# Optimization experiments

Measured on AMD Instinct MI355X. Metric: run time of the kernel, lower is better.

The kernel has to match this reference:

```python
import jax, jax.numpy as jnp
import numpy as np

B, N, D, H = 4, 8192, 1024, 16
HD = D // H  # head dim 64
EPS = 1e-5


def setup_inputs() -> dict:
    key = jax.random.key(0)
    ks = jax.random.split(key, 12)
    s = 1.0 / np.sqrt(D)
    return {
        "query": jax.random.normal(ks[0], (B, N, D), jnp.float32),
        "Wq": jax.random.normal(ks[1], (D, D), jnp.float32) * s,
        "bq": jax.random.normal(ks[2], (D,), jnp.float32) * 0.01,
        "Wk": jax.random.normal(ks[3], (D, D), jnp.float32) * s,
        "bk": jax.random.normal(ks[4], (D,), jnp.float32) * 0.01,
        "Wv": jax.random.normal(ks[5], (D, D), jnp.float32) * s,
        "bv": jax.random.normal(ks[6], (D,), jnp.float32) * 0.01,
        "Wu": jax.random.normal(ks[7], (D, D), jnp.float32) * s,
        "bu": jax.random.normal(ks[8], (D,), jnp.float32) * 0.01,
        "Wo": jax.random.normal(ks[9], (D, D), jnp.float32) * s,
        "bo": jax.random.normal(ks[10], (D,), jnp.float32) * 0.01,
        "ln_w": jnp.ones((D,), jnp.float32),
        "ln_b": jnp.zeros((D,), jnp.float32),
    }


def _abs_clamp(t, min_mag=0.01, max_mag=100.0):
    return jnp.clip(jnp.abs(t), min_mag, max_mag) * jnp.sign(t)


def _heads(x):  # [b, n, h*d] -> [b, h, n, d]
    b, n, _ = x.shape
    return x.reshape(b, n, H, HD).transpose(0, 2, 1, 3)


def reference(query, Wq, bq, Wk, bk, Wv, bv, Wu, bu, Wo, bo, ln_w, ln_b):
    q = jax.nn.relu(_heads(query @ Wq + bq))  # [b,h,n,d]
    k = jax.nn.relu(_heads(query @ Wk + bk))
    v = _heads(query @ Wv + bv)
    u = query @ Wu + bu  # [b,n,D]
    # global linear-attention reduction: kv[b,h,d,e] = sum_n k v
    kv = jnp.einsum('bhnd,bhne->bhde', k, v)
    kv = _abs_clamp(kv)
    out = jnp.einsum('bhnd,bhde->bhne', q, kv)  # [b,h,n,d]
    out = out.transpose(0, 2, 1, 3).reshape(query.shape)  # [b,n,D]
    # LayerNorm over last dim
    mu = jnp.mean(out, axis=-1, keepdims=True)
    var = jnp.var(out, axis=-1, keepdims=True)
    out = (out - mu) * jax.lax.rsqrt(var + EPS) * ln_w + ln_b
    out = u * out
    return out @ Wo + bo
```

## Files before the change

### kernel.cpp

```cpp
#include <hip/hip_runtime.h>

#define M_TOT 32768

typedef float f32x4 __attribute__((ext_vector_type(4)));
typedef short s16x8 __attribute__((ext_vector_type(8)));

#define AS1(p) ((__attribute__((address_space(1))) void*)(p))
#define AS3(p) ((__attribute__((address_space(3))) void*)(p))

#define BARRIER() asm volatile("s_barrier" ::: "memory")
#define VMCNT4() asm volatile("s_waitcnt vmcnt(4)" ::: "memory")
#define VMCNT2() asm volatile("s_waitcnt vmcnt(2)" ::: "memory")
#define VMCNT0() asm volatile("s_waitcnt vmcnt(0)" ::: "memory")

__device__ __forceinline__ short f2bf(float f) {
    unsigned u = __builtin_bit_cast(unsigned, f);
    u += 0x7fffu + ((u >> 16) & 1u);
    return (short)(u >> 16);
}
__device__ __forceinline__ float bf2f(short s) {
    unsigned u = ((unsigned)(unsigned short)s) << 16;
    return __builtin_bit_cast(float, u);
}

__global__ void conv_x(const float* __restrict__ x, short* __restrict__ y) {
    const size_t nchunk = (size_t)M_TOT * 1024 / 8;
    const size_t stride = (size_t)gridDim.x * blockDim.x;
    for (size_t c = (size_t)blockIdx.x * blockDim.x + threadIdx.x; c < nchunk; c += stride) {
        const float4* src = (const float4*)(x + c * 8);
        float4 a = src[0], b = src[1];
        s16x8 r;
        r[0] = f2bf(a.x); r[1] = f2bf(a.y); r[2] = f2bf(a.z); r[3] = f2bf(a.w);
        r[4] = f2bf(b.x); r[5] = f2bf(b.y); r[6] = f2bf(b.z); r[7] = f2bf(b.w);
        *(s16x8*)(y + c * 8) = r;
    }
}

__global__ __launch_bounds__(256) void conv_w(const float* __restrict__ Wq,
                                              const float* __restrict__ Wk,
                                              const float* __restrict__ Wv,
                                              const float* __restrict__ Wu,
                                              const float* __restrict__ Wo,
                                              short* __restrict__ Wcat) {
    __shared__ float t[64][65];
    const int b = blockIdx.x;
    const int mat = b >> 8;
    const int kt = (b >> 4) & 15, nt = b & 15;
    const int k0 = kt << 6, n0 = nt << 6;
    const float* W = (mat == 0) ? Wq : (mat == 1) ? Wk : (mat == 2) ? Wv
                   : (mat == 3) ? Wu : Wo;
    const int rr = threadIdx.x >> 4;
    const int cc = threadIdx.x & 15;
    #pragma unroll
    for (int p = 0; p < 4; ++p) {
        const int row = p * 16 + rr;
        const float4 v = *(const float4*)(W + (size_t)(k0 + row) * 1024 + n0 + cc * 4);
        t[row][cc * 4 + 0] = v.x; t[row][cc * 4 + 1] = v.y;
        t[row][cc * 4 + 2] = v.z; t[row][cc * 4 + 3] = v.w;
    }
    __syncthreads();
    #pragma unroll
    for (int p = 0; p < 4; ++p) {
        const int nr = p * 16 + rr;
        short4 r;
        r.x = f2bf(t[cc * 4 + 0][nr]); r.y = f2bf(t[cc * 4 + 1][nr]);
        r.z = f2bf(t[cc * 4 + 2][nr]); r.w = f2bf(t[cc * 4 + 3][nr]);
        *(short4*)(Wcat + (size_t)(mat * 1024 + n0 + nr) * 1024 + k0 + cc * 4) = r;
    }
}

__global__ void conv_bias(const float* __restrict__ bq, const float* __restrict__ bk,
                          const float* __restrict__ bv, const float* __restrict__ bu,
                          const float* __restrict__ bo, float* __restrict__ bcat) {
    const int i = blockIdx.x * 256 + threadIdx.x;
    const float* b = (i < 1024) ? bq : (i < 2048) ? bk : (i < 3072) ? bv
                   : (i < 4096) ? bu : bo;
    bcat[i] = b[i & 1023];
}

template <int MODE>
__global__ __launch_bounds__(512, 2) void gemm8(
        const short* __restrict__ A, const short* __restrict__ W,
        const float* __restrict__ bias,
        short* __restrict__ qb, short* __restrict__ ktb,
        short* __restrict__ vtb, short* __restrict__ ub,
        float* __restrict__ outb) {
    extern __shared__ char lds[];
    const int tid = threadIdx.x;
    const int wave = tid >> 6, lane = tid & 63;
    const int r16 = lane & 15, g = lane >> 4;
    const int moff = (wave >> 2) << 7;
    const int noff = (wave & 3) << 6;

    const int nwg = (MODE == 0) ? 2048 : 512;
    const int NB = (MODE == 0) ? 16 : 4;
    const int bid = blockIdx.x;
    const int swz = (bid & 7) * (nwg >> 3) + (bid >> 3);
    const int mblk = swz / NB, nblk = swz % NB;
    const int row0 = mblk << 8, col0 = nblk << 8;

    const int rswz = r16 & 7;
    const int ck0 = (g ^ rswz) << 4;
    const int ck1 = ((4 + g) ^ rswz) << 4;
    const int rowbA = (moff + r16) << 7;
    const int rowbB = (noff + r16) << 7;

    const char* baseA = (const char*)A + (size_t)(row0 + wave * 8 + (lane >> 3)) * 2048
                        + (((lane & 7) ^ ((lane >> 3) & 7)) << 4);
    const char* baseB = (const char*)W + (size_t)(col0 + wave * 8 + (lane >> 3)) * 2048
                        + (((lane & 7) ^ ((lane >> 3) & 7)) << 4);

#define STG(BASE, J, T, DST)                                                   \
    __builtin_amdgcn_global_load_lds(                                          \
        AS1((BASE) + (size_t)(J) * 131072 + (size_t)(T) * 128),                \
        AS3((DST) + (J) * 8192 + wave * 1024), 16, 0, 0)

#define RDA(V, M, BUFA) {                                                      \
    (V)[0] = *(const s16x8*)((BUFA) + rowbA + (M) * 2048 + ck0);               \
    (V)[1] = *(const s16x8*)((BUFA) + rowbA + (M) * 2048 + ck1); }

#define RDB(V, N, BUFB) {                                                      \
    (V)[0] = *(const s16x8*)((BUFB) + rowbB + (N) * 2048 + ck0);               \
    (V)[1] = *(const s16x8*)((BUFB) + rowbB + (N) * 2048 + ck1); }

#define MF16(P, A0, A1)                                                        \
    _Pragma("unroll") for (int kk = 0; kk < 2; ++kk)                           \
        _Pragma("unroll") for (int n = 0; n < 4; ++n) {                        \
            acc[2*(P)][n]   = __builtin_amdgcn_mfma_f32_16x16x32_bf16((A0)[kk], bfr[n][kk], acc[2*(P)][n], 0, 0, 0);   \
            acc[2*(P)+1][n] = __builtin_amdgcn_mfma_f32_16x16x32_bf16((A1)[kk], bfr[n][kk], acc[2*(P)+1][n], 0, 0, 0); \
        }

#define TILE(T, DOSTAGE, TRmid, TRend) {                                       \
    char* bA_ = lds + ((T) & 1) * 65536; char* bB_ = bA_ + 32768;              \
    char* sA_ = lds + (((T) + 1) & 1) * 65536; char* sB_ = sA_ + 32768;        \
    s16x8 a0[2], a1[2], a2[2], a3[2];                                          \
    if (DOSTAGE) { STG(baseB, 0, (T) + 1, sB_); STG(baseB, 1, (T) + 1, sB_);   \
                   STG(baseB, 2, (T) + 1, sB_); STG(baseB, 3, (T) + 1, sB_); } \
    _Pragma("unroll") for (int n = 0; n < 4; ++n) RDB(bfr[n], n, bB_);         \
    RDA(a0, 0, bA_); RDA(a1, 1, bA_); RDA(a2, 2, bA_); RDA(a3, 3, bA_);        \
    __builtin_amdgcn_s_setprio(1);                                             \
    MF16(0, a0, a1); MF16(1, a2, a3);                                          \
    __builtin_amdgcn_s_setprio(0);                                             \
    TRmid; BARRIER();                                                          \
    if (DOSTAGE) { STG(baseA, 0, (T) + 1, sA_); STG(baseA, 2, (T) + 1, sA_);   \
                   STG(baseA, 1, (T) + 1, sA_); STG(baseA, 3, (T) + 1, sA_); } \
    RDA(a0, 4, bA_); RDA(a1, 5, bA_); RDA(a2, 6, bA_); RDA(a3, 7, bA_);        \
    __builtin_amdgcn_s_setprio(1);                                             \
    MF16(2, a0, a1); MF16(3, a2, a3);                                          \
    __builtin_amdgcn_s_setprio(0);                                             \
    TRend; BARRIER(); }

    f32x4 acc[8][4] = {};
    s16x8 bfr[4][2];

    STG(baseB, 0, 0, lds + 32768); STG(baseB, 1, 0, lds + 32768);
    STG(baseB, 2, 0, lds + 32768); STG(baseB, 3, 0, lds + 32768);
    STG(baseA, 0, 0, lds);         STG(baseA, 2, 0, lds);
    STG(baseA, 1, 0, lds);         STG(baseA, 3, 0, lds);
    VMCNT2();
    BARRIER();

    #pragma unroll 1
    for (int t = 0; t < 15; ++t) TILE(t, true, VMCNT4(), VMCNT2());
    TILE(15, false, VMCNT0(), (void)0);

    const int rj = (lane >> 4) << 2;
    if (MODE == 1) {
        #pragma unroll
        for (int n = 0; n < 4; ++n) {
            const int gn = col0 + noff + n * 16 + r16;
            const float bv = bias[gn];
            #pragma unroll
            for (int m = 0; m < 8; ++m) {
                const int gm0 = row0 + moff + m * 16 + rj;
                #pragma unroll
                for (int j = 0; j < 4; ++j)
                    outb[(size_t)(gm0 + j) * 1024 + gn] = acc[m][n][j] + bv;
            }
        }
    } else {
        const int seg = col0 >> 10;
        if (seg == 0 || seg == 3) {
            short* dst = (seg == 0) ? qb : ub;
            const bool do_relu = (seg == 0);
            #pragma unroll
            for (int n = 0; n < 4; ++n) {
                const int gn = col0 + noff + n * 16 + r16;
                const int f = gn & 1023;
                const float bv = bias[gn];
                #pragma unroll
                for (int m = 0; m < 8; ++m) {
                    const int gm0 = row0 + moff + m * 16 + rj;
                    #pragma unroll
                    for (int j = 0; j < 4; ++j) {
                        float val = acc[m][n][j] + bv;
                        if (do_relu) val = fmaxf(val, 0.0f);
                        dst[(size_t)(gm0 + j) * 1024 + f] = f2bf(val);
                    }
                }
            }
        } else {
            short* dst = (seg == 1) ? ktb : vtb;
            const bool do_relu = (seg == 1);
            #pragma unroll
            for (int n = 0; n < 4; ++n) {
                const int gn = col0 + noff + n * 16 + r16;
                const int hd = gn & 1023;
                const float bv = bias[gn];
                #pragma unroll
                for (int m = 0; m < 8; ++m) {
                    const int gm0 = row0 + moff + m * 16 + rj;
                    const int b = gm0 >> 13;
                    const int ntok = gm0 & 8191;
                    float v0 = acc[m][n][0] + bv, v1 = acc[m][n][1] + bv;
                    float v2 = acc[m][n][2] + bv, v3 = acc[m][n][3] + bv;
                    if (do_relu) {
                        v0 = fmaxf(v0, 0.0f); v1 = fmaxf(v1, 0.0f);
                        v2 = fmaxf(v2, 0.0f); v3 = fmaxf(v3, 0.0f);
                    }
                    short4 pk;
                    pk.x = f2bf(v0); pk.y = f2bf(v1); pk.z = f2bf(v2); pk.w = f2bf(v3);
                    *(short4*)(dst + ((size_t)(b * 1024 + hd)) * 8192 + ntok) = pk;
                }
            }
        }
    }
#undef TILE
#undef MF16
#undef RDB
#undef RDA
#undef STG
}

__global__ __launch_bounds__(256) void kv_partial(const short* __restrict__ ktb,
                                                  const short* __restrict__ vtb,
                                                  float* __restrict__ kvp) {
    __shared__ float red[4][4096];
    const int slice = blockIdx.x;
    const int bh = blockIdx.y;
    const int wave = threadIdx.x >> 6, lane = threadIdx.x & 63;
    const int r16 = lane & 15;
    const short* kb = ktb + (size_t)bh * 64 * 8192;
    const short* vb = vtb + (size_t)bh * 64 * 8192;
    const int n0 = (slice << 10) + (wave << 8);
    f32x4 acc[4][4] = {};
    for (int s = 0; s < 8; ++s) {
        const int nk = n0 + (s << 5) + ((lane >> 4) << 3);
        s16x8 af[4], bf[4];
        #pragma unroll
        for (int m = 0; m < 4; ++m) af[m] = *(const s16x8*)(kb + (size_t)(m * 16 + r16) * 8192 + nk);
        #pragma unroll
        for (int n = 0; n < 4; ++n) bf[n] = *(const s16x8*)(vb + (size_t)(n * 16 + r16) * 8192 + nk);
        #pragma unroll
        for (int m = 0; m < 4; ++m)
            #pragma unroll
            for (int n = 0; n < 4; ++n)
                acc[m][n] = __builtin_amdgcn_mfma_f32_16x16x32_bf16(af[m], bf[n], acc[m][n], 0, 0, 0);
    }
    const int rj = (lane >> 4) << 2;
    #pragma unroll
    for (int m = 0; m < 4; ++m)
        #pragma unroll
        for (int n = 0; n < 4; ++n)
            #pragma unroll
            for (int j = 0; j < 4; ++j)
                red[wave][(m * 16 + rj + j) * 64 + n * 16 + r16] = acc[m][n][j];
    __syncthreads();
    float* dst = kvp + ((size_t)slice * 64 + bh) * 4096;
    const int i0 = threadIdx.x * 16;
    #pragma unroll
    for (int e = 0; e < 16; e += 4) {
        f32x4 a0 = *(const f32x4*)&red[0][i0 + e];
        f32x4 a1 = *(const f32x4*)&red[1][i0 + e];
        f32x4 a2 = *(const f32x4*)&red[2][i0 + e];
        f32x4 a3 = *(const f32x4*)&red[3][i0 + e];
        *(f32x4*)&dst[i0 + e] = (a0 + a1) + (a2 + a3);
    }
}

__global__ void kv_reduce(const float* __restrict__ kvp, short* __restrict__ kvt) {
    const int bh = blockIdx.x;
    for (int i = threadIdx.x; i < 4096; i += 256) {
        float s = 0.0f;
        #pragma unroll
        for (int sl = 0; sl < 8; ++sl)
            s += kvp[((size_t)sl * 64 + bh) * 4096 + i];
        float a = fabsf(s);
        float cmag = fminf(fmaxf(a, 0.01f), 100.0f);
        float r = (s > 0.0f) ? cmag : ((s < 0.0f) ? -cmag : 0.0f);
        const int d = i >> 6, e = i & 63;
        kvt[(size_t)bh * 4096 + e * 64 + d] = f2bf(r);
    }
}

__global__ __launch_bounds__(256) void qkv_ln(const short* __restrict__ qb,
                                              const short* __restrict__ kvt,
                                              const short* __restrict__ ub,
                                              const float* __restrict__ lnw,
                                              const float* __restrict__ lnb,
                                              short* __restrict__ yb) {
    __shared__ short tr[4][1024];
    const int wave = threadIdx.x >> 6, lane = threadIdx.x & 63;
    const int r16 = lane & 15, g = lane >> 4;
    const size_t rowB = (size_t)blockIdx.x * 64 + wave * 16;
    const int bh0 = (int)((rowB >> 13) << 4);
    const short* qrow = qb + (rowB + r16) * 1024 + g * 8;

    float s[4] = {0, 0, 0, 0}, sq[4] = {0, 0, 0, 0};
    for (int h = 0; h < 16; ++h) {
        const short* kvb = kvt + (size_t)(bh0 + h) * 4096 + g * 8;
        f32x4 a4[4] = {};
        #pragma unroll
        for (int kk = 0; kk < 2; ++kk) {
            const s16x8 af = *(const s16x8*)(qrow + h * 64 + kk * 32);
            #pragma unroll
            for (int n = 0; n < 4; ++n) {
                const s16x8 bf = *(const s16x8*)(kvb + (n * 16 + r16) * 64 + kk * 32);
                a4[n] = __builtin_amdgcn_mfma_f32_16x16x32_bf16(af, bf, a4[n], 0, 0, 0);
            }
        }
        #pragma unroll
        for (int n = 0; n < 4; ++n)
            #pragma unroll
            for (int j = 0; j < 4; ++j) {
                const float v = a4[n][j];
                s[j] += v; sq[j] += v * v;
            }
    }
    #pragma unroll
    for (int j = 0; j < 4; ++j) {
        #pragma unroll
        for (int mk = 1; mk < 16; mk <<= 1) {
            s[j] += __shfl_xor(s[j], mk);
            sq[j] += __shfl_xor(sq[j], mk);
        }
    }
    float mu[4], rs[4];
    #pragma unroll
    for (int j = 0; j < 4; ++j) {
        mu[j] = s[j] * (1.0f / 1024.0f);
        const float var = sq[j] * (1.0f / 1024.0f) - mu[j] * mu[j];
        rs[j] = rsqrtf(var + 1e-5f);
    }

    short* trw = &tr[wave][0];
    const int rdr = lane >> 3;
    const int c0 = (lane & 7) * 8;
    for (int h = 0; h < 16; ++h) {
        const short* kvb = kvt + (size_t)(bh0 + h) * 4096 + g * 8;
        f32x4 a4[4] = {};
        #pragma unroll
        for (int kk = 0; kk < 2; ++kk) {
            const s16x8 af = *(const s16x8*)(qrow + h * 64 + kk * 32);
            #pragma unroll
            for (int n = 0; n < 4; ++n) {
                const s16x8 bf = *(const s16x8*)(kvb + (n * 16 + r16) * 64 + kk * 32);
                a4[n] = __builtin_amdgcn_mfma_f32_16x16x32_bf16(af, bf, a4[n], 0, 0, 0);
            }
        }
        #pragma unroll
        for (int n = 0; n < 4; ++n) {
            const float lw = lnw[h * 64 + n * 16 + r16];
            const float lb = lnb[h * 64 + n * 16 + r16];
            #pragma unroll
            for (int j = 0; j < 4; ++j) {
                const float val = (a4[n][j] - mu[j]) * rs[j] * lw + lb;
                trw[(g * 4 + j) * 64 + ((n ^ g) * 16 + r16)] = f2bf(val);
            }
        }
        #pragma unroll
        for (int p = 0; p < 2; ++p) {
            const int r = rdr + p * 8;
            const s16x8 t = *(const s16x8*)&trw[r * 64 + (((c0 >> 4) ^ (r >> 2)) * 16) + (c0 & 15)];
            const s16x8 uu = *(const s16x8*)(ub + (rowB + r) * 1024 + h * 64 + c0);
            s16x8 o;
            #pragma unroll
            for (int e = 0; e < 8; ++e)
                o[e] = f2bf(bf2f(t[e]) * bf2f(uu[e]));
            *(s16x8*)(yb + (rowB + r) * 1024 + h * 64 + c0) = o;
        }
    }
}

extern "C" void kernel_launch(void* const* d_in, const int* in_sizes, int n_in,
                              void* d_out, int out_size, void* d_ws, size_t ws_size,
                              hipStream_t stream) {
    (void)in_sizes; (void)n_in; (void)out_size;
    const float* query = (const float*)d_in[0];
    const float* Wq = (const float*)d_in[1];
    const float* bq = (const float*)d_in[2];
    const float* Wk = (const float*)d_in[3];
    const float* bk = (const float*)d_in[4];
    const float* Wv = (const float*)d_in[5];
    const float* bv = (const float*)d_in[6];
    const float* Wu = (const float*)d_in[7];
    const float* bu = (const float*)d_in[8];
    const float* Wo = (const float*)d_in[9];
    const float* bo = (const float*)d_in[10];
    const float* lnw = (const float*)d_in[11];
    const float* lnb = (const float*)d_in[12];
    float* out = (float*)d_out;
    char* ws = (char*)d_ws;
    if (ws_size < 380129280u) return;

    short* Xb   = (short*)(ws);
    short* Wcat = (short*)(ws + 67108864);
    float* bcat = (float*)(ws + 77594624);
    short* qb   = (short*)(ws + 77615104);
    short* ktb  = (short*)(ws + 144723968);
    short* vtb  = (short*)(ws + 211832832);
    short* ub   = (short*)(ws + 278941696);
    float* kvp  = (float*)(ws + 346050560);
    short* kvt  = (short*)(ws + 379604992);
    short* yb   = Xb;

    hipFuncSetAttribute(reinterpret_cast<const void*>(&gemm8<0>),
                        hipFuncAttributeMaxDynamicSharedMemorySize, 131072);
    hipFuncSetAttribute(reinterpret_cast<const void*>(&gemm8<1>),
                        hipFuncAttributeMaxDynamicSharedMemorySize, 131072);

    conv_x<<<2048, 256, 0, stream>>>(query, Xb);
    conv_w<<<1280, 256, 0, stream>>>(Wq, Wk, Wv, Wu, Wo, Wcat);
    conv_bias<<<20, 256, 0, stream>>>(bq, bk, bv, bu, bo, bcat);
    gemm8<0><<<2048, 512, 131072, stream>>>(Xb, Wcat, bcat, qb, ktb, vtb, ub, nullptr);
    kv_partial<<<dim3(8, 64), 256, 0, stream>>>(ktb, vtb, kvp);
    kv_reduce<<<64, 256, 0, stream>>>(kvp, kvt);
    qkv_ln<<<512, 256, 0, stream>>>(qb, kvt, ub, lnw, lnb, yb);
    gemm8<1><<<512, 512, 131072, stream>>>(yb, Wcat + (size_t)4096 * 1024, bcat + 4096,
                                           nullptr, nullptr, nullptr, nullptr, out);
}
```

Before: 537.4 us.

## Restructure GEMM main loop into four k-split phases with interleaved staging

The GEMM inner loop now splits each 64-wide K tile into four phases by M-half and K-half, holding only one K-slice of A and B fragments in registers at a time. Each phase issues its LDS reads and two global-to-LDS stage loads, then waits on a barrier and lgkmcnt(0) before running 16 MFMAs under raised priority. The goal is to spread global loads more evenly across the tile and to cut fragment register pressure. In exchange it adds two extra barriers per tile and full LDS waits that may expose read latency.

```diff
diff --git a/kernel.cpp b/kernel.cpp
--- a/kernel.cpp
+++ b/kernel.cpp
@@ -9,7 +9,7 @@
 #define AS3(p) ((__attribute__((address_space(3))) void*)(p))
 
 #define BARRIER() asm volatile("s_barrier" ::: "memory")
-#define VMCNT4() asm volatile("s_waitcnt vmcnt(4)" ::: "memory")
+#define LGKM0()  asm volatile("s_waitcnt lgkmcnt(0)" ::: "memory")
 #define VMCNT2() asm volatile("s_waitcnt vmcnt(2)" ::: "memory")
 #define VMCNT0() asm volatile("s_waitcnt vmcnt(0)" ::: "memory")
 
@@ -79,7 +79,7 @@
 }
 
 template <int MODE>
-__global__ __launch_bounds__(512, 2) void gemm8(
+__global__ __launch_bounds__(512, 2) void gemm9(
         const short* __restrict__ A, const short* __restrict__ W,
         const float* __restrict__ bias,
         short* __restrict__ qb, short* __restrict__ ktb,
@@ -115,54 +115,58 @@
         AS1((BASE) + (size_t)(J) * 131072 + (size_t)(T) * 128),                \
         AS3((DST) + (J) * 8192 + wave * 1024), 16, 0, 0)
 
-#define RDA(V, M, BUFA) {                                                      \
-    (V)[0] = *(const s16x8*)((BUFA) + rowbA + (M) * 2048 + ck0);               \
-    (V)[1] = *(const s16x8*)((BUFA) + rowbA + (M) * 2048 + ck1); }
-
-#define RDB(V, N, BUFB) {                                                      \
-    (V)[0] = *(const s16x8*)((BUFB) + rowbB + (N) * 2048 + ck0);               \
-    (V)[1] = *(const s16x8*)((BUFB) + rowbB + (N) * 2048 + ck1); }
-
-#define MF16(P, A0, A1)                                                        \
-    _Pragma("unroll") for (int kk = 0; kk < 2; ++kk)                           \
-        _Pragma("unroll") for (int n = 0; n < 4; ++n) {                        \
-            acc[2*(P)][n]   = __builtin_amdgcn_mfma_f32_16x16x32_bf16((A0)[kk], bfr[n][kk], acc[2*(P)][n], 0, 0, 0);   \
-            acc[2*(P)+1][n] = __builtin_amdgcn_mfma_f32_16x16x32_bf16((A1)[kk], bfr[n][kk], acc[2*(P)+1][n], 0, 0, 0); \
-        }
-
-#define TILE(T, DOSTAGE, TRmid, TRend) {                                       \
-    char* bA_ = lds + ((T) & 1) * 65536; char* bB_ = bA_ + 32768;              \
-    char* sA_ = lds + (((T) + 1) & 1) * 65536; char* sB_ = sA_ + 32768;        \
-    s16x8 a0[2], a1[2], a2[2], a3[2];                                          \
-    if (DOSTAGE) { STG(baseB, 0, (T) + 1, sB_); STG(baseB, 1, (T) + 1, sB_);   \
-                   STG(baseB, 2, (T) + 1, sB_); STG(baseB, 3, (T) + 1, sB_); } \
-    _Pragma("unroll") for (int n = 0; n < 4; ++n) RDB(bfr[n], n, bB_);         \
-    RDA(a0, 0, bA_); RDA(a1, 1, bA_); RDA(a2, 2, bA_); RDA(a3, 3, bA_);        \
+#define RA(M, QM, CK) (*(const s16x8*)(bA_ + rowbA + (QM) * 8192 + (M) * 2048 + (CK)))
+#define RB(N, CK)     (*(const s16x8*)(bB_ + rowbB + (N) * 2048 + (CK)))
+
+#define PH(QM, CK, FRESHB, DOST, SBASE, J1, J2, SDST, WAITOP) {                \
+    afr[0] = RA(0, QM, CK); afr[1] = RA(1, QM, CK);                            \
+    afr[2] = RA(2, QM, CK); afr[3] = RA(3, QM, CK);                            \
+    if (FRESHB) { bfr[0] = RB(0, CK); bfr[1] = RB(1, CK);                      \
+                  bfr[2] = RB(2, CK); bfr[3] = RB(3, CK); }                    \
+    if (DOST) { STG(SBASE, J1, tt + 1, SDST); STG(SBASE, J2, tt + 1, SDST); }  \
+    BARRIER();                                                                 \
+    LGKM0();                                                                   \
+    __builtin_amdgcn_sched_barrier(0);                                         \
     __builtin_amdgcn_s_setprio(1);                                             \
-    MF16(0, a0, a1); MF16(1, a2, a3);                                          \
+    _Pragma("unroll") for (int m = 0; m < 4; ++m)                              \
+        _Pragma("unroll") for (int n = 0; n < 4; ++n)                          \
+            acc[(QM) * 4 + m][n] = __builtin_amdgcn_mfma_f32_16x16x32_bf16(    \
+                afr[m], bfr[n], acc[(QM) * 4 + m][n], 0, 0, 0);                \
     __builtin_amdgcn_s_setprio(0);                                             \
-    TRmid; BARRIER();                                                          \
-    if (DOSTAGE) { STG(baseA, 0, (T) + 1, sA_); STG(baseA, 2, (T) + 1, sA_);   \
-                   STG(baseA, 1, (T) + 1, sA_); STG(baseA, 3, (T) + 1, sA_); } \
-    RDA(a0, 4, bA_); RDA(a1, 5, bA_); RDA(a2, 6, bA_); RDA(a3, 7, bA_);        \
-    __builtin_amdgcn_s_setprio(1);                                             \
-    MF16(2, a0, a1); MF16(3, a2, a3);                                          \
-    __builtin_amdgcn_s_setprio(0);                                             \
-    TRend; BARRIER(); }
+    WAITOP;                                                                    \
+    BARRIER(); }
 
     f32x4 acc[8][4] = {};
-    s16x8 bfr[4][2];
-
-    STG(baseB, 0, 0, lds + 32768); STG(baseB, 1, 0, lds + 32768);
-    STG(baseB, 2, 0, lds + 32768); STG(baseB, 3, 0, lds + 32768);
-    STG(baseA, 0, 0, lds);         STG(baseA, 2, 0, lds);
-    STG(baseA, 1, 0, lds);         STG(baseA, 3, 0, lds);
+    s16x8 afr[4], bfr[4];
+
+    {
+        const int tt = -1;
+        STG(baseB, 0, tt + 1, lds + 32768); STG(baseB, 1, tt + 1, lds + 32768);
+        STG(baseB, 2, tt + 1, lds + 32768); STG(baseB, 3, tt + 1, lds + 32768);
+        STG(baseA, 0, tt + 1, lds);         STG(baseA, 2, tt + 1, lds);
+        STG(baseA, 1, tt + 1, lds);         STG(baseA, 3, tt + 1, lds);
+    }
     VMCNT2();
     BARRIER();
 
     #pragma unroll 1
-    for (int t = 0; t < 15; ++t) TILE(t, true, VMCNT4(), VMCNT2());
-    TILE(15, false, VMCNT0(), (void)0);
+    for (int tt = 0; tt < 15; ++tt) {
+        char* bA_ = lds + (tt & 1) * 65536; char* bB_ = bA_ + 32768;
+        char* sA_ = lds + ((tt + 1) & 1) * 65536; char* sB_ = sA_ + 32768;
+        PH(0, ck0, true,  true, baseB, 0, 1, sB_, VMCNT2());
+        PH(1, ck0, false, true, baseB, 2, 3, sB_, (void)0);
+        PH(0, ck1, true,  true, baseA, 0, 2, sA_, (void)0);
+        PH(1, ck1, false, true, baseA, 1, 3, sA_, VMCNT2());
+    }
+    {
+        const int tt = 15;
+        char* bA_ = lds + (tt & 1) * 65536; char* bB_ = bA_ + 32768;
+        char* sA_ = nullptr; char* sB_ = nullptr; (void)sA_; (void)sB_;
+        PH(0, ck0, true,  false, baseB, 0, 1, sB_, VMCNT0());
+        PH(1, ck0, false, false, baseB, 2, 3, sB_, (void)0);
+        PH(0, ck1, true,  false, baseA, 0, 2, sA_, (void)0);
+        PH(1, ck1, false, false, baseA, 1, 3, sA_, (void)0);
+    }
 
     const int rj = (lane >> 4) << 2;
     if (MODE == 1) {
@@ -225,10 +229,9 @@
             }
         }
     }
-#undef TILE
-#undef MF16
-#undef RDB
-#undef RDA
+#undef PH
+#undef RB
+#undef RA
 #undef STG
 }
 
@@ -414,18 +417,18 @@
     short* kvt  = (short*)(ws + 379604992);
     short* yb   = Xb;
 
-    hipFuncSetAttribute(reinterpret_cast<const void*>(&gemm8<0>),
+    hipFuncSetAttribute(reinterpret_cast<const void*>(&gemm9<0>),
                         hipFuncAttributeMaxDynamicSharedMemorySize, 131072);
-    hipFuncSetAttribute(reinterpret_cast<const void*>(&gemm8<1>),
+    hipFuncSetAttribute(reinterpret_cast<const void*>(&gemm9<1>),
                         hipFuncAttributeMaxDynamicSharedMemorySize, 131072);
 
     conv_x<<<2048, 256, 0, stream>>>(query, Xb);
     conv_w<<<1280, 256, 0, stream>>>(Wq, Wk, Wv, Wu, Wo, Wcat);
     conv_bias<<<20, 256, 0, stream>>>(bq, bk, bv, bu, bo, bcat);
-    gemm8<0><<<2048, 512, 131072, stream>>>(Xb, Wcat, bcat, qb, ktb, vtb, ub, nullptr);
+    gemm9<0><<<2048, 512, 131072, stream>>>(Xb, Wcat, bcat, qb, ktb, vtb, ub, nullptr);
     kv_partial<<<dim3(8, 64), 256, 0, stream>>>(ktb, vtb, kvp);
     kv_reduce<<<64, 256, 0, stream>>>(kvp, kvt);
     qkv_ln<<<512, 256, 0, stream>>>(qb, kvt, ub, lnw, lnb, yb);
-    gemm8<1><<<512, 512, 131072, stream>>>(yb, Wcat + (size_t)4096 * 1024, bcat + 4096,
+    gemm9<1><<<512, 512, 131072, stream>>>(yb, Wcat + (size_t)4096 * 1024, bcat + 4096,
                                            nullptr, nullptr, nullptr, nullptr, out);
 }
```

Result: no change. 542.2 us (+0.9%).

## Triple-buffer GEMM with K=32 tiles and merge prep kernels into one launch

Applied to the files above, without the earlier changes.

The main GEMM changes from a two-stage pipeline with K=64 tiles (128 KB LDS) to a three-stage ring of K=32 tiles (96 KB LDS), prefetching two tiles ahead. It uses a new XOR swizzle and a single barrier per tile. The three conversion kernels (x, weights, bias) are merged into one prep launch to cut launch overhead. Risks: twice as many barriers over the K loop, and lower MFMA work per synchronization.

```diff
diff --git a/kernel.cpp b/kernel.cpp
--- a/kernel.cpp
+++ b/kernel.cpp
@@ -10,7 +10,6 @@
 
 #define BARRIER() asm volatile("s_barrier" ::: "memory")
 #define VMCNT4() asm volatile("s_waitcnt vmcnt(4)" ::: "memory")
-#define VMCNT2() asm volatile("s_waitcnt vmcnt(2)" ::: "memory")
 #define VMCNT0() asm volatile("s_waitcnt vmcnt(0)" ::: "memory")
 
 __device__ __forceinline__ short f2bf(float f) {
@@ -23,63 +22,61 @@
     return __builtin_bit_cast(float, u);
 }
 
-__global__ void conv_x(const float* __restrict__ x, short* __restrict__ y) {
-    const size_t nchunk = (size_t)M_TOT * 1024 / 8;
-    const size_t stride = (size_t)gridDim.x * blockDim.x;
-    for (size_t c = (size_t)blockIdx.x * blockDim.x + threadIdx.x; c < nchunk; c += stride) {
-        const float4* src = (const float4*)(x + c * 8);
-        float4 a = src[0], b = src[1];
-        s16x8 r;
-        r[0] = f2bf(a.x); r[1] = f2bf(a.y); r[2] = f2bf(a.z); r[3] = f2bf(a.w);
-        r[4] = f2bf(b.x); r[5] = f2bf(b.y); r[6] = f2bf(b.z); r[7] = f2bf(b.w);
-        *(s16x8*)(y + c * 8) = r;
-    }
-}
-
-__global__ __launch_bounds__(256) void conv_w(const float* __restrict__ Wq,
-                                              const float* __restrict__ Wk,
-                                              const float* __restrict__ Wv,
-                                              const float* __restrict__ Wu,
-                                              const float* __restrict__ Wo,
-                                              short* __restrict__ Wcat) {
+__global__ __launch_bounds__(256) void prep(const float* __restrict__ x, short* __restrict__ y,
+                                            const float* __restrict__ Wq, const float* __restrict__ Wk,
+                                            const float* __restrict__ Wv, const float* __restrict__ Wu,
+                                            const float* __restrict__ Wo, short* __restrict__ Wcat,
+                                            const float* __restrict__ bq, const float* __restrict__ bk,
+                                            const float* __restrict__ bv, const float* __restrict__ bu,
+                                            const float* __restrict__ bo, float* __restrict__ bcat) {
     __shared__ float t[64][65];
-    const int b = blockIdx.x;
-    const int mat = b >> 8;
-    const int kt = (b >> 4) & 15, nt = b & 15;
-    const int k0 = kt << 6, n0 = nt << 6;
-    const float* W = (mat == 0) ? Wq : (mat == 1) ? Wk : (mat == 2) ? Wv
-                   : (mat == 3) ? Wu : Wo;
-    const int rr = threadIdx.x >> 4;
-    const int cc = threadIdx.x & 15;
-    #pragma unroll
-    for (int p = 0; p < 4; ++p) {
-        const int row = p * 16 + rr;
-        const float4 v = *(const float4*)(W + (size_t)(k0 + row) * 1024 + n0 + cc * 4);
-        t[row][cc * 4 + 0] = v.x; t[row][cc * 4 + 1] = v.y;
-        t[row][cc * 4 + 2] = v.z; t[row][cc * 4 + 3] = v.w;
-    }
-    __syncthreads();
-    #pragma unroll
-    for (int p = 0; p < 4; ++p) {
-        const int nr = p * 16 + rr;
-        short4 r;
-        r.x = f2bf(t[cc * 4 + 0][nr]); r.y = f2bf(t[cc * 4 + 1][nr]);
-        r.z = f2bf(t[cc * 4 + 2][nr]); r.w = f2bf(t[cc * 4 + 3][nr]);
-        *(short4*)(Wcat + (size_t)(mat * 1024 + n0 + nr) * 1024 + k0 + cc * 4) = r;
-    }
-}
-
-__global__ void conv_bias(const float* __restrict__ bq, const float* __restrict__ bk,
-                          const float* __restrict__ bv, const float* __restrict__ bu,
-                          const float* __restrict__ bo, float* __restrict__ bcat) {
-    const int i = blockIdx.x * 256 + threadIdx.x;
-    const float* b = (i < 1024) ? bq : (i < 2048) ? bk : (i < 3072) ? bv
-                   : (i < 4096) ? bu : bo;
-    bcat[i] = b[i & 1023];
+    const int blk = blockIdx.x;
+    if (blk < 2048) {
+        const size_t nchunk = (size_t)M_TOT * 1024 / 8;
+        const size_t stride = (size_t)2048 * 256;
+        for (size_t c = (size_t)blk * 256 + threadIdx.x; c < nchunk; c += stride) {
+            const float4* src = (const float4*)(x + c * 8);
+            float4 a = src[0], b = src[1];
+            s16x8 r;
+            r[0] = f2bf(a.x); r[1] = f2bf(a.y); r[2] = f2bf(a.z); r[3] = f2bf(a.w);
+            r[4] = f2bf(b.x); r[5] = f2bf(b.y); r[6] = f2bf(b.z); r[7] = f2bf(b.w);
+            *(s16x8*)(y + c * 8) = r;
+        }
+    } else if (blk < 3328) {
+        const int b = blk - 2048;
+        const int mat = b >> 8;
+        const int kt = (b >> 4) & 15, nt = b & 15;
+        const int k0 = kt << 6, n0 = nt << 6;
+        const float* W = (mat == 0) ? Wq : (mat == 1) ? Wk : (mat == 2) ? Wv
+                       : (mat == 3) ? Wu : Wo;
+        const int rr = threadIdx.x >> 4;
+        const int cc = threadIdx.x & 15;
+        #pragma unroll
+        for (int p = 0; p < 4; ++p) {
+            const int row = p * 16 + rr;
+            const float4 v = *(const float4*)(W + (size_t)(k0 + row) * 1024 + n0 + cc * 4);
+            t[row][cc * 4 + 0] = v.x; t[row][cc * 4 + 1] = v.y;
+            t[row][cc * 4 + 2] = v.z; t[row][cc * 4 + 3] = v.w;
+        }
+        __syncthreads();
+        #pragma unroll
+        for (int p = 0; p < 4; ++p) {
+            const int nr = p * 16 + rr;
+            short4 r;
+            r.x = f2bf(t[cc * 4 + 0][nr]); r.y = f2bf(t[cc * 4 + 1][nr]);
+            r.z = f2bf(t[cc * 4 + 2][nr]); r.w = f2bf(t[cc * 4 + 3][nr]);
+            *(short4*)(Wcat + (size_t)(mat * 1024 + n0 + nr) * 1024 + k0 + cc * 4) = r;
+        }
+    } else {
+        const int i = (blk - 3328) * 256 + threadIdx.x;
+        const float* b = (i < 1024) ? bq : (i < 2048) ? bk : (i < 3072) ? bv
+                       : (i < 4096) ? bu : bo;
+        bcat[i] = b[i & 1023];
+    }
 }
 
 template <int MODE>
-__global__ __launch_bounds__(512, 2) void gemm8(
+__global__ __launch_bounds__(512, 2) void gemmD(
         const short* __restrict__ A, const short* __restrict__ W,
         const float* __restrict__ bias,
         short* __restrict__ qb, short* __restrict__ ktb,
@@ -99,70 +96,57 @@
     const int mblk = swz / NB, nblk = swz % NB;
     const int row0 = mblk << 8, col0 = nblk << 8;
 
-    const int rswz = r16 & 7;
-    const int ck0 = (g ^ rswz) << 4;
-    const int ck1 = ((4 + g) ^ rswz) << 4;
-    const int rowbA = (moff + r16) << 7;
-    const int rowbB = (noff + r16) << 7;
-
-    const char* baseA = (const char*)A + (size_t)(row0 + wave * 8 + (lane >> 3)) * 2048
-                        + (((lane & 7) ^ ((lane >> 3) & 7)) << 4);
-    const char* baseB = (const char*)W + (size_t)(col0 + wave * 8 + (lane >> 3)) * 2048
-                        + (((lane & 7) ^ ((lane >> 3) & 7)) << 4);
+    const int ck = ((g ^ (r16 & 3) ^ ((r16 >> 2) & 3)) << 4);
+    const int rowbA = (moff + r16) << 6;
+    const int rowbB = (noff + r16) << 6;
+
+    const int srow = tid >> 2;
+    const int scs = (((tid & 3) ^ (srow & 3) ^ ((srow >> 2) & 3)) << 4);
+    const char* Agl = (const char*)A + (size_t)(row0 + srow) * 2048 + scs;
+    const char* Bgl = (const char*)W + (size_t)(col0 + srow) * 2048 + scs;
 
 #define STG(BASE, J, T, DST)                                                   \
     __builtin_amdgcn_global_load_lds(                                          \
-        AS1((BASE) + (size_t)(J) * 131072 + (size_t)(T) * 128),                \
-        AS3((DST) + (J) * 8192 + wave * 1024), 16, 0, 0)
-
-#define RDA(V, M, BUFA) {                                                      \
-    (V)[0] = *(const s16x8*)((BUFA) + rowbA + (M) * 2048 + ck0);               \
-    (V)[1] = *(const s16x8*)((BUFA) + rowbA + (M) * 2048 + ck1); }
-
-#define RDB(V, N, BUFB) {                                                      \
-    (V)[0] = *(const s16x8*)((BUFB) + rowbB + (N) * 2048 + ck0);               \
-    (V)[1] = *(const s16x8*)((BUFB) + rowbB + (N) * 2048 + ck1); }
-
-#define MF16(P, A0, A1)                                                        \
-    _Pragma("unroll") for (int kk = 0; kk < 2; ++kk)                           \
-        _Pragma("unroll") for (int n = 0; n < 4; ++n) {                        \
-            acc[2*(P)][n]   = __builtin_amdgcn_mfma_f32_16x16x32_bf16((A0)[kk], bfr[n][kk], acc[2*(P)][n], 0, 0, 0);   \
-            acc[2*(P)+1][n] = __builtin_amdgcn_mfma_f32_16x16x32_bf16((A1)[kk], bfr[n][kk], acc[2*(P)+1][n], 0, 0, 0); \
-        }
-
-#define TILE(T, DOSTAGE, TRmid, TRend) {                                       \
-    char* bA_ = lds + ((T) & 1) * 65536; char* bB_ = bA_ + 32768;              \
-    char* sA_ = lds + (((T) + 1) & 1) * 65536; char* sB_ = sA_ + 32768;        \
-    s16x8 a0[2], a1[2], a2[2], a3[2];                                          \
-    if (DOSTAGE) { STG(baseB, 0, (T) + 1, sB_); STG(baseB, 1, (T) + 1, sB_);   \
-                   STG(baseB, 2, (T) + 1, sB_); STG(baseB, 3, (T) + 1, sB_); } \
-    _Pragma("unroll") for (int n = 0; n < 4; ++n) RDB(bfr[n], n, bB_);         \
-    RDA(a0, 0, bA_); RDA(a1, 1, bA_); RDA(a2, 2, bA_); RDA(a3, 3, bA_);        \
+        AS1((BASE) + (size_t)(J) * 262144 + (size_t)(T) * 64),                 \
+        AS3((DST) + (J) * 8192 + tid * 16), 16, 0, 0)
+
+#define TILE(T, RB, SB, DOSTAGE, WAIT) {                                       \
+    char* rb_ = lds + (RB) * 32768;                                            \
+    char* sb_ = lds + (SB) * 32768;                                            \
+    if (DOSTAGE) { STG(Agl, 0, (T) + 2, sb_); STG(Agl, 1, (T) + 2, sb_);       \
+                   STG(Bgl, 0, (T) + 2, sb_ + 16384);                          \
+                   STG(Bgl, 1, (T) + 2, sb_ + 16384); }                        \
+    s16x8 bfr[4], afr[8];                                                      \
+    _Pragma("unroll") for (int n = 0; n < 4; ++n)                              \
+        bfr[n] = *(const s16x8*)(rb_ + 16384 + rowbB + n * 1024 + ck);         \
+    _Pragma("unroll") for (int m = 0; m < 8; ++m)                              \
+        afr[m] = *(const s16x8*)(rb_ + rowbA + m * 1024 + ck);                 \
     __builtin_amdgcn_s_setprio(1);                                             \
-    MF16(0, a0, a1); MF16(1, a2, a3);                                          \
+    _Pragma("unroll") for (int m = 0; m < 8; ++m)                              \
+        _Pragma("unroll") for (int n = 0; n < 4; ++n)                          \
+            acc[m][n] = __builtin_amdgcn_mfma_f32_16x16x32_bf16(               \
+                afr[m], bfr[n], acc[m][n], 0, 0, 0);                           \
     __builtin_amdgcn_s_setprio(0);                                             \
-    TRmid; BARRIER();                                                          \
-    if (DOSTAGE) { STG(baseA, 0, (T) + 1, sA_); STG(baseA, 2, (T) + 1, sA_);   \
-                   STG(baseA, 1, (T) + 1, sA_); STG(baseA, 3, (T) + 1, sA_); } \
-    RDA(a0, 4, bA_); RDA(a1, 5, bA_); RDA(a2, 6, bA_); RDA(a3, 7, bA_);        \
-    __builtin_amdgcn_s_setprio(1);                                             \
-    MF16(2, a0, a1); MF16(3, a2, a3);                                          \
-    __builtin_amdgcn_s_setprio(0);                                             \
-    TRend; BARRIER(); }
+    WAIT;                                                                      \
+    BARRIER(); }
 
     f32x4 acc[8][4] = {};
-    s16x8 bfr[4][2];
-
-    STG(baseB, 0, 0, lds + 32768); STG(baseB, 1, 0, lds + 32768);
-    STG(baseB, 2, 0, lds + 32768); STG(baseB, 3, 0, lds + 32768);
-    STG(baseA, 0, 0, lds);         STG(baseA, 2, 0, lds);
-    STG(baseA, 1, 0, lds);         STG(baseA, 3, 0, lds);
-    VMCNT2();
+
+    STG(Agl, 0, 0, lds); STG(Agl, 1, 0, lds);
+    STG(Bgl, 0, 0, lds + 16384); STG(Bgl, 1, 0, lds + 16384);
+    STG(Agl, 0, 1, lds + 32768); STG(Agl, 1, 1, lds + 32768);
+    STG(Bgl, 0, 1, lds + 49152); STG(Bgl, 1, 1, lds + 49152);
+    VMCNT4();
     BARRIER();
 
     #pragma unroll 1
-    for (int t = 0; t < 15; ++t) TILE(t, true, VMCNT4(), VMCNT2());
-    TILE(15, false, VMCNT0(), (void)0);
+    for (int t = 0; t < 30; t += 3) {
+        TILE(t + 0, 0, 2, true, VMCNT4());
+        TILE(t + 1, 1, 0, true, VMCNT4());
+        TILE(t + 2, 2, 1, true, VMCNT4());
+    }
+    TILE(30, 0, 0, false, VMCNT0());
+    TILE(31, 1, 1, false, (void)0);
 
     const int rj = (lane >> 4) << 2;
     if (MODE == 1) {
@@ -226,9 +210,6 @@
         }
     }
 #undef TILE
-#undef MF16
-#undef RDB
-#undef RDA
 #undef STG
 }
 
@@ -414,18 +395,17 @@
     short* kvt  = (short*)(ws + 379604992);
     short* yb   = Xb;
 
-    hipFuncSetAttribute(reinterpret_cast<const void*>(&gemm8<0>),
-                        hipFuncAttributeMaxDynamicSharedMemorySize, 131072);
-    hipFuncSetAttribute(reinterpret_cast<const void*>(&gemm8<1>),
-                        hipFuncAttributeMaxDynamicSharedMemorySize, 131072);
-
-    conv_x<<<2048, 256, 0, stream>>>(query, Xb);
-    conv_w<<<1280, 256, 0, stream>>>(Wq, Wk, Wv, Wu, Wo, Wcat);
-    conv_bias<<<20, 256, 0, stream>>>(bq, bk, bv, bu, bo, bcat);
-    gemm8<0><<<2048, 512, 131072, stream>>>(Xb, Wcat, bcat, qb, ktb, vtb, ub, nullptr);
+    hipFuncSetAttribute(reinterpret_cast<const void*>(&gemmD<0>),
+                        hipFuncAttributeMaxDynamicSharedMemorySize, 98304);
+    hipFuncSetAttribute(reinterpret_cast<const void*>(&gemmD<1>),
+                        hipFuncAttributeMaxDynamicSharedMemorySize, 98304);
+
+    prep<<<3348, 256, 0, stream>>>(query, Xb, Wq, Wk, Wv, Wu, Wo, Wcat,
+                                   bq, bk, bv, bu, bo, bcat);
+    gemmD<0><<<2048, 512, 98304, stream>>>(Xb, Wcat, bcat, qb, ktb, vtb, ub, nullptr);
     kv_partial<<<dim3(8, 64), 256, 0, stream>>>(ktb, vtb, kvp);
     kv_reduce<<<64, 256, 0, stream>>>(kvp, kvt);
     qkv_ln<<<512, 256, 0, stream>>>(qb, kvt, ub, lnw, lnb, yb);
-    gemm8<1><<<512, 512, 131072, stream>>>(yb, Wcat + (size_t)4096 * 1024, bcat + 4096,
-                                           nullptr, nullptr, nullptr, nullptr, out);
-}
+    gemmD<1><<<512, 512, 98304, stream>>>(yb, Wcat + (size_t)4096 * 1024, bcat + 4096,
+                                          nullptr, nullptr, nullptr, nullptr, out);
+}
```

Result: slower. 553.4 us (+3.0%).
